# Optimization experiments

Hardware: AMD Instinct MI355X
Metric: run time of the kernel (lower is better)

The kernel has to match this reference:

```python
import jax, jax.numpy as jnp
import numpy as np
import math

N_HEADS = 4
N_KV_GROUPS = 1
HEAD_DIM = 256
SLIDING_WINDOW = 512
ROPE_BASE = 1000000.0
EPS = 1e-6


def _rmsnorm(x, gamma):
    # normalize over last dim (head_dim), torch nn.RMSNorm semantics
    ms = jnp.mean(jnp.square(x), axis=-1, keepdims=True)
    return x * jax.lax.rsqrt(ms + EPS) * gamma


def _rope_tables(T, head_dim, dtype):
    inv_freq = 1.0 / (ROPE_BASE ** (jnp.arange(0, head_dim, 2, dtype=jnp.float32) / head_dim))
    t = jnp.arange(T, dtype=jnp.float32)
    freqs = jnp.outer(t, inv_freq)          # [T, head_dim/2]
    return jnp.cos(freqs).astype(dtype), jnp.sin(freqs).astype(dtype)


def _apply_rope(x, cos, sin):
    # x: [B, T, H, hd]; cos/sin: [T, hd/2] broadcast as [1, T, 1, hd/2]
    x0 = x[..., 0::2]
    x1 = x[..., 1::2]
    c = cos[None, :, None, :]
    s = sin[None, :, None, :]
    even = x0 * c - x1 * s
    odd = x0 * s + x1 * c
    return jnp.stack((even, odd), axis=-1).reshape(x.shape)


def setup_inputs() -> dict:
    key = jax.random.key(0)
    ks = jax.random.split(key, 5)
    B, T, C = 2, 4096, 1024
    scale = 0.02
    return {
        "x": jax.random.normal(ks[0], (B, T, C), dtype=jnp.float32),
        "Wq": jax.random.normal(ks[1], (C, C), dtype=jnp.float32) * scale,
        "Wk": jax.random.normal(ks[2], (N_KV_GROUPS * HEAD_DIM, C), dtype=jnp.float32) * scale,
        "Wv": jax.random.normal(ks[3], (N_KV_GROUPS * HEAD_DIM, C), dtype=jnp.float32) * scale,
        "Wo": jax.random.normal(ks[4], (C, C), dtype=jnp.float32) * scale,
        "q_gamma": jnp.ones((HEAD_DIM,), dtype=jnp.float32),
        "k_gamma": jnp.ones((HEAD_DIM,), dtype=jnp.float32),
    }


def reference(x, Wq, Wk, Wv, Wo, q_gamma, k_gamma):
    B, T, C = x.shape
    H, G, hd = N_HEADS, N_KV_GROUPS, HEAD_DIM
    rep = H // G

    q = (x @ Wq.T).reshape(B, T, H, hd)
    k = (x @ Wk.T).reshape(B, T, G, hd)
    v = (x @ Wv.T).reshape(B, T, G, hd)

    q = _rmsnorm(q, q_gamma)
    k = _rmsnorm(k, k_gamma)

    cos, sin = _rope_tables(T, hd, q.dtype)
    q = _apply_rope(q, cos, sin)
    k = _apply_rope(k, cos, sin)

    q = q.transpose(0, 2, 1, 3)                 # [B, H, T, hd]
    k = k.transpose(0, 2, 1, 3)                 # [B, G, T, hd]
    v = v.transpose(0, 2, 1, 3)
    k = jnp.repeat(k, rep, axis=1)              # [B, H, T, hd]
    v = jnp.repeat(v, rep, axis=1)

    scores = jnp.einsum("bhqd,bhkd->bhqk", q, k) / math.sqrt(hd)
    i = jnp.arange(T)[:, None]
    j = jnp.arange(T)[None, :]
    allowed = (j <= i) & (j >= i - SLIDING_WINDOW)   # causal sliding window
    scores = jnp.where(allowed, scores, -jnp.inf)
    attn = jax.nn.softmax(scores, axis=-1)
    out = jnp.einsum("bhqk,bhkd->bhqd", attn, v)     # [B, H, T, hd]
    out = out.transpose(0, 2, 1, 3).reshape(B, T, C)
    return out @ Wo.T
```

## Files before the change

kernel.cpp:

```cpp
#include <hip/hip_runtime.h>
#include <cstdint>
#include <cstddef>

#define T_SEQ 4096
#define NB    2
#define CDIM  1024
#define HD    256
#define NH    4

typedef __attribute__((ext_vector_type(8))) __bf16 bf16x8;
typedef __attribute__((ext_vector_type(4))) __bf16 bf16x4;
typedef __attribute__((ext_vector_type(4))) float  floatx4;

__device__ __forceinline__ floatx4 mfma16(bf16x8 a, bf16x8 b, floatx4 c) {
  return __builtin_amdgcn_mfma_f32_16x16x32_bf16(a, b, c, 0, 0, 0);
}

__device__ __forceinline__ void gl2lds16(const void* g, void* l) {
  __builtin_amdgcn_global_load_lds(
      (__attribute__((address_space(1))) void*)g,
      (__attribute__((address_space(3))) void*)l, 16, 0, 0);
}

__global__ void cvt_f32_bf16(const float* __restrict__ in,
                             __bf16* __restrict__ out, int n4) {
  int i = blockIdx.x * 256 + threadIdx.x;
  if (i < n4) {
    float4 v = ((const float4*)in)[i];
    bf16x4 o;
    o[0] = (__bf16)v.x; o[1] = (__bf16)v.y; o[2] = (__bf16)v.z; o[3] = (__bf16)v.w;
    *(bf16x4*)&out[(size_t)i * 4] = o;
  }
}

template <typename OutT>
__global__ __launch_bounds__(256) void gemm_bt(const __bf16* __restrict__ A,
                                               const __bf16* __restrict__ B,
                                               OutT* __restrict__ C,
                                               int M, int N, int K) {
  __shared__ __bf16 As[128 * 64];
  __shared__ __bf16 Bs[128 * 64];
  const int tid  = threadIdx.x;
  const int lane = tid & 63;
  const int wave = tid >> 6;
  const int wm = wave >> 1, wn = wave & 1;
  const int lrow = lane & 15, quad = lane >> 4;
  const int bm = blockIdx.y, bn = blockIdx.x;

  const __bf16* gA = A + (size_t)(bm * 128) * K;
  const __bf16* gB = B + (size_t)(bn * 128) * K;
  const int arow = tid >> 3;
  const int acol = ((tid & 7) ^ ((tid >> 3) & 7)) * 8;
  const int l7 = lrow & 7;

  floatx4 acc[4][4] = {};

  for (int kt = 0; kt < K; kt += 64) {
#pragma unroll
    for (int i = 0; i < 4; ++i)
      gl2lds16(gA + (size_t)(i * 32 + arow) * K + kt + acol, &As[i * 2048 + tid * 8]);
#pragma unroll
    for (int i = 0; i < 4; ++i)
      gl2lds16(gB + (size_t)(i * 32 + arow) * K + kt + acol, &Bs[i * 2048 + tid * 8]);
    __syncthreads();
#pragma unroll
    for (int kk = 0; kk < 2; ++kk) {
      bf16x8 af[4], bfr[4];
#pragma unroll
      for (int mi = 0; mi < 4; ++mi)
        af[mi] = *(const bf16x8*)&As[(wm * 64 + mi * 16 + lrow) * 64 +
                                     ((kk * 4 + quad) ^ l7) * 8];
#pragma unroll
      for (int ni = 0; ni < 4; ++ni)
        bfr[ni] = *(const bf16x8*)&Bs[(wn * 64 + ni * 16 + lrow) * 64 +
                                      ((kk * 4 + quad) ^ l7) * 8];
#pragma unroll
      for (int mi = 0; mi < 4; ++mi)
#pragma unroll
        for (int ni = 0; ni < 4; ++ni)
          acc[mi][ni] = mfma16(af[mi], bfr[ni], acc[mi][ni]);
    }
    __syncthreads();
  }

  const int row0 = bm * 128 + wm * 64;
  const int col0 = bn * 128 + wn * 64;
#pragma unroll
  for (int mi = 0; mi < 4; ++mi)
#pragma unroll
    for (int ni = 0; ni < 4; ++ni)
#pragma unroll
      for (int r = 0; r < 4; ++r) {
        int row = row0 + mi * 16 + quad * 4 + r;
        int col = col0 + ni * 16 + lrow;
        C[(size_t)row * N + col] = (OutT)acc[mi][ni][r];
      }
}

__global__ __launch_bounds__(256) void rmsrope(const __bf16* __restrict__ qkv,
                                               const float* __restrict__ qg,
                                               const float* __restrict__ kg,
                                               __bf16* __restrict__ qr,
                                               __bf16* __restrict__ kr,
                                               __bf16* __restrict__ vt) {
  __shared__ __bf16 Ls[64 * 256];
  if (blockIdx.x >= 10240) {
    const int vb = blockIdx.x - 10240;
    const int b = vb >> 6, tt = vb & 63;
    const int tid = threadIdx.x;
    const __bf16* src = qkv + ((size_t)(b * 4096 + tt * 64)) * 1536 + 1280;
#pragma unroll
    for (int i = 0; i < 8; ++i)
      gl2lds16(src + (size_t)(i * 8 + (tid >> 5)) * 1536 + (tid & 31) * 8,
               &Ls[i * 2048 + tid * 8]);
    __syncthreads();
    __bf16 buf[64];
#pragma unroll
    for (int i = 0; i < 64; ++i) buf[i] = Ls[i * 256 + tid];
    __bf16* dst = vt + ((size_t)(b * 256 + tid)) * T_SEQ + tt * 64;
#pragma unroll
    for (int i = 0; i < 8; ++i)
      *(bf16x8*)&dst[i * 8] = *(const bf16x8*)&buf[i * 8];
    return;
  }

  const int inst = blockIdx.x * 4 + (threadIdx.x >> 6);
  const int lane = threadIdx.x & 63;
  const int row = inst / 5, which = inst - row * 5;
  const int b = row >> 12, t = row & 4095;

  const int srcoff = (which < 4) ? which * 256 : 1024;
  const __bf16* src = qkv + (size_t)row * 1536 + srcoff;
  bf16x4 xv = *(const bf16x4*)&src[lane * 4];

  float x0 = (float)xv[0], x1 = (float)xv[1], x2 = (float)xv[2], x3 = (float)xv[3];
  float ss = x0 * x0 + x1 * x1 + x2 * x2 + x3 * x3;
#pragma unroll
  for (int off = 32; off >= 1; off >>= 1) ss += __shfl_xor(ss, off);
  const float rms = rsqrtf(ss * (1.0f / 256.0f) + 1e-6f);

  const float* g = (which < 4) ? qg : kg;
  const float4 gv = *(const float4*)&g[lane * 4];
  float y0 = x0 * rms * gv.x, y1 = x1 * rms * gv.y;
  float y2 = x2 * rms * gv.z, y3 = x3 * rms * gv.w;

  const float c_log2 = -19.931568569324174f / 128.0f;
  int p0 = lane * 2, p1 = lane * 2 + 1;
  float a0 = (float)t * exp2f((float)p0 * c_log2);
  float a1 = (float)t * exp2f((float)p1 * c_log2);
  float s0, c0, s1, c1;
  sincosf(a0, &s0, &c0);
  sincosf(a1, &s1, &c1);
  bf16x4 ov;
  ov[0] = (__bf16)(y0 * c0 - y1 * s0);
  ov[1] = (__bf16)(y0 * s0 + y1 * c0);
  ov[2] = (__bf16)(y2 * c1 - y3 * s1);
  ov[3] = (__bf16)(y2 * s1 + y3 * c1);

  __bf16* dst = (which < 4)
      ? qr + ((size_t)((b * NH + which) * T_SEQ) + t) * 256
      : kr + ((size_t)(b * T_SEQ) + t) * 256;
  *(bf16x4*)&dst[lane * 4] = ov;
}

__global__ __launch_bounds__(256, 2) void attn(const __bf16* __restrict__ qr,
                                               const __bf16* __restrict__ kr,
                                               const __bf16* __restrict__ vt,
                                               __bf16* __restrict__ ao) {
  __shared__ __bf16 Ks[64 * 256];
  __shared__ __bf16 Ps[64 * 64];

  const int bid = blockIdx.x;
  const int qi = bid & 63, h = (bid >> 6) & 3, b = bid >> 8;
  const int tid = threadIdx.x, wave = tid >> 6, lane = tid & 63;
  const int wq = wave & 1, wk = wave >> 1;
  const int lrow = lane & 15, quad = lane >> 4;
  const int l7 = lrow & 7;

  const __bf16* Q = qr + (size_t)((b * NH + h) * T_SEQ) * 256;
  const __bf16* K = kr + (size_t)(b * T_SEQ) * 256;
  const __bf16* V = vt + (size_t)(b * 256) * T_SEQ;

  const int qbase = qi * 64;

  bf16x8 qf[2][8];
#pragma unroll
  for (int qt = 0; qt < 2; ++qt)
#pragma unroll
    for (int c = 0; c < 8; ++c)
      qf[qt][c] = *(const bf16x8*)&Q[(size_t)(qbase + wq * 32 + qt * 16 + lrow) * 256 +
                                     c * 32 + quad * 8];

  bf16x8 onesv;
#pragma unroll
  for (int j = 0; j < 8; ++j) onesv[j] = (__bf16)1.0f;

  floatx4 o[2][8] = {};
  floatx4 lm[2] = {};

  const int jt0 = (qi >= 8) ? qi - 8 : 0;
  const int jt1 = qi;

  {
    const __bf16* Kt = K + (size_t)(jt0 * 64) * 256;
#pragma unroll
    for (int i = 0; i < 8; ++i)
      gl2lds16(Kt + (size_t)(i * 8 + (tid >> 5)) * 256 +
                   ((tid & 31) ^ ((tid >> 5) & 7)) * 8,
               &Ks[i * 2048 + tid * 8]);
  }

  for (int jt = jt0; jt <= jt1; ++jt) {
    __syncthreads();

    floatx4 s[2][2] = {};
#pragma unroll
    for (int c = 0; c < 8; ++c)
#pragma unroll
      for (int k16 = 0; k16 < 2; ++k16) {
        bf16x8 kf = *(const bf16x8*)&Ks[(wk * 32 + k16 * 16 + lrow) * 256 +
                                        ((c * 4 + quad) ^ l7) * 8];
#pragma unroll
        for (int qt = 0; qt < 2; ++qt)
          s[k16][qt] = mfma16(kf, qf[qt][c], s[k16][qt]);
      }

    const bool full = (jt < qi) && (jt >= qi - 7);

    const float C1 = 0.09016844005556021f;
    const float C2 = 23.083120654223415f;
#pragma unroll
    for (int k16 = 0; k16 < 2; ++k16)
#pragma unroll
      for (int qt = 0; qt < 2; ++qt) {
        bf16x4 pk;
#pragma unroll
        for (int r = 0; r < 4; ++r) {
          float v = s[k16][qt][r];
          if (!full) {
            const int jk = jt * 64 + wk * 32 + k16 * 16 + quad * 4 + r;
            const int iq = qbase + wq * 32 + qt * 16 + lrow;
            v = ((jk <= iq) && (jk + 512 >= iq)) ? v : -1e30f;
          }
          pk[r] = (__bf16)exp2f(v * C1 - C2);
        }
        const int q = wq * 32 + qt * 16 + lrow;
        const int chunk = (wk * 4 + k16 * 2 + (quad >> 1)) ^ l7;
        *(bf16x4*)((char*)Ps + q * 128 + chunk * 16 + (quad & 1) * 8) = pk;
      }
    __syncthreads();

    if (jt < jt1) {
      const __bf16* Kt = K + (size_t)((jt + 1) * 64) * 256;
#pragma unroll
      for (int i = 0; i < 8; ++i)
        gl2lds16(Kt + (size_t)(i * 8 + (tid >> 5)) * 256 +
                     ((tid & 31) ^ ((tid >> 5) & 7)) * 8,
                 &Ks[i * 2048 + tid * 8]);
    }

    bf16x8 pf[2][2];
#pragma unroll
    for (int qt = 0; qt < 2; ++qt)
#pragma unroll
      for (int kc = 0; kc < 2; ++kc) {
        const int q = wq * 32 + qt * 16 + lrow;
        pf[qt][kc] = *(const bf16x8*)((char*)Ps + q * 128 +
                                      ((kc * 4 + quad) ^ l7) * 16);
      }

#pragma unroll
    for (int qt = 0; qt < 2; ++qt) {
      lm[qt] = mfma16(pf[qt][0], onesv, lm[qt]);
      lm[qt] = mfma16(pf[qt][1], onesv, lm[qt]);
    }

#pragma unroll
    for (int n = 0; n < 8; ++n)
#pragma unroll
      for (int kc = 0; kc < 2; ++kc) {
        bf16x8 vf = *(const bf16x8*)&V[(size_t)(wk * 128 + n * 16 + lrow) * T_SEQ +
                                       jt * 64 + kc * 32 + quad * 8];
        o[0][n] = mfma16(pf[0][kc], vf, o[0][n]);
        o[1][n] = mfma16(pf[1][kc], vf, o[1][n]);
      }
  }

#pragma unroll
  for (int qt = 0; qt < 2; ++qt)
#pragma unroll
    for (int r = 0; r < 4; ++r) {
      const float rl = 1.0f / lm[qt][r];
      const int tg = qbase + wq * 32 + qt * 16 + quad * 4 + r;
#pragma unroll
      for (int n = 0; n < 8; ++n)
        ao[((size_t)(b * T_SEQ + tg)) * CDIM + h * 256 + wk * 128 + n * 16 + lrow] =
            (__bf16)(o[qt][n][r] * rl);
    }
}

extern "C" void kernel_launch(void* const* d_in, const int* in_sizes, int n_in,
                              void* d_out, int out_size, void* d_ws, size_t ws_size,
                              hipStream_t stream) {
  const float* x  = (const float*)d_in[0];
  const float* Wq = (const float*)d_in[1];
  const float* Wk = (const float*)d_in[2];
  const float* Wv = (const float*)d_in[3];
  const float* Wo = (const float*)d_in[4];
  const float* qg = (const float*)d_in[5];
  const float* kg = (const float*)d_in[6];
  float* out = (float*)d_out;

  const size_t M = (size_t)NB * T_SEQ;
  char* ws = (char*)d_ws;
  __bf16* xb  = (__bf16*)ws; ws += M * CDIM * 2;
  __bf16* wb  = (__bf16*)ws; ws += (size_t)1536 * CDIM * 2;
  __bf16* wob = (__bf16*)ws; ws += (size_t)CDIM * CDIM * 2;
  __bf16* qkv = (__bf16*)ws; ws += M * 1536 * 2;
  __bf16* qr  = (__bf16*)ws; ws += M * CDIM * 2;
  __bf16* kr  = (__bf16*)ws; ws += M * HD * 2;
  __bf16* vt  = (__bf16*)ws; ws += M * HD * 2;
  __bf16* ao  = (__bf16*)ws;

  cvt_f32_bf16<<<8192, 256, 0, stream>>>(x, xb, 2097152);
  cvt_f32_bf16<<<1024, 256, 0, stream>>>(Wq, wb, 262144);
  cvt_f32_bf16<<<256,  256, 0, stream>>>(Wk, wb + 1024 * 1024, 65536);
  cvt_f32_bf16<<<256,  256, 0, stream>>>(Wv, wb + 1280 * 1024, 65536);
  cvt_f32_bf16<<<1024, 256, 0, stream>>>(Wo, wob, 262144);

  gemm_bt<__bf16><<<dim3(12, 64), 256, 0, stream>>>(xb, wb, qkv, 8192, 1536, 1024);

  rmsrope<<<10368, 256, 0, stream>>>(qkv, qg, kg, qr, kr, vt);

  attn<<<NB * NH * (T_SEQ / 64), 256, 0, stream>>>(qr, kr, vt, ao);

  gemm_bt<float><<<dim3(8, 64), 256, 0, stream>>>(ao, wob, out, 8192, 1024, 1024);
}
```

Before: 235.8 us.

## Double-buffer attention K/P tiles, prefetch V early, fuse conversions, fast sincos

The attention kernel now double-buffers the K and P tiles in LDS and prefetches K two tiles ahead. V fragments are loaded into registers at the top of each iteration so global latency overlaps the QK MFMAs. The five fp32-to-bf16 conversion launches are merged into one kernel, and the RoPE sincosf calls are replaced with the __sinf/__cosf intrinsics. The costs are doubled LDS use, higher register pressure from holding vf, and reduced trig accuracy at large angles (t up to 4096).

```diff
diff --git a/kernel.cpp b/kernel.cpp
--- a/kernel.cpp
+++ b/kernel.cpp
@@ -22,15 +22,27 @@
       (__attribute__((address_space(3))) void*)l, 16, 0, 0);
 }
 
-__global__ void cvt_f32_bf16(const float* __restrict__ in,
-                             __bf16* __restrict__ out, int n4) {
+__global__ __launch_bounds__(256) void cvt_all(const float* __restrict__ x,
+                                               const float* __restrict__ wq,
+                                               const float* __restrict__ wk,
+                                               const float* __restrict__ wv,
+                                               const float* __restrict__ wo,
+                                               __bf16* __restrict__ xb,
+                                               __bf16* __restrict__ wb,
+                                               __bf16* __restrict__ wob) {
   int i = blockIdx.x * 256 + threadIdx.x;
-  if (i < n4) {
-    float4 v = ((const float4*)in)[i];
-    bf16x4 o;
-    o[0] = (__bf16)v.x; o[1] = (__bf16)v.y; o[2] = (__bf16)v.z; o[3] = (__bf16)v.w;
-    *(bf16x4*)&out[(size_t)i * 4] = o;
-  }
+  const float* src;
+  __bf16* dst;
+  int off;
+  if (i < 2097152)      { src = x;  dst = xb;            off = i; }
+  else if (i < 2359296) { src = wq; dst = wb;            off = i - 2097152; }
+  else if (i < 2424832) { src = wk; dst = wb + 1048576;  off = i - 2359296; }
+  else if (i < 2490368) { src = wv; dst = wb + 1310720;  off = i - 2424832; }
+  else                  { src = wo; dst = wob;           off = i - 2490368; }
+  float4 v = ((const float4*)src)[off];
+  bf16x4 o;
+  o[0] = (__bf16)v.x; o[1] = (__bf16)v.y; o[2] = (__bf16)v.z; o[3] = (__bf16)v.w;
+  *(bf16x4*)&dst[(size_t)off * 4] = o;
 }
 
 template <typename OutT>
@@ -148,9 +160,8 @@
   int p0 = lane * 2, p1 = lane * 2 + 1;
   float a0 = (float)t * exp2f((float)p0 * c_log2);
   float a1 = (float)t * exp2f((float)p1 * c_log2);
-  float s0, c0, s1, c1;
-  sincosf(a0, &s0, &c0);
-  sincosf(a1, &s1, &c1);
+  float s0 = __sinf(a0), c0 = __cosf(a0);
+  float s1 = __sinf(a1), c1 = __cosf(a1);
   bf16x4 ov;
   ov[0] = (__bf16)(y0 * c0 - y1 * s0);
   ov[1] = (__bf16)(y0 * s0 + y1 * c0);
@@ -167,8 +178,8 @@
                                                const __bf16* __restrict__ kr,
                                                const __bf16* __restrict__ vt,
                                                __bf16* __restrict__ ao) {
-  __shared__ __bf16 Ks[64 * 256];
-  __shared__ __bf16 Ps[64 * 64];
+  __shared__ __bf16 Ks[2][64 * 256];
+  __shared__ __bf16 Ps[2][64 * 64];
 
   const int bid = blockIdx.x;
   const int qi = bid & 63, h = (bid >> 6) & 3, b = bid >> 8;
@@ -207,18 +218,36 @@
     for (int i = 0; i < 8; ++i)
       gl2lds16(Kt + (size_t)(i * 8 + (tid >> 5)) * 256 +
                    ((tid & 31) ^ ((tid >> 5) & 7)) * 8,
-               &Ks[i * 2048 + tid * 8]);
-  }
+               &Ks[jt0 & 1][i * 2048 + tid * 8]);
+  }
+  if (jt1 > jt0) {
+    const __bf16* Kt = K + (size_t)((jt0 + 1) * 64) * 256;
+#pragma unroll
+    for (int i = 0; i < 8; ++i)
+      gl2lds16(Kt + (size_t)(i * 8 + (tid >> 5)) * 256 +
+                   ((tid & 31) ^ ((tid >> 5) & 7)) * 8,
+               &Ks[(jt0 + 1) & 1][i * 2048 + tid * 8]);
+  }
+  __syncthreads();
 
   for (int jt = jt0; jt <= jt1; ++jt) {
-    __syncthreads();
+    const __bf16* Kb = Ks[jt & 1];
+    __bf16* Pb = Ps[jt & 1];
+
+    bf16x8 vf[8][2];
+#pragma unroll
+    for (int n = 0; n < 8; ++n)
+#pragma unroll
+      for (int kc = 0; kc < 2; ++kc)
+        vf[n][kc] = *(const bf16x8*)&V[(size_t)(wk * 128 + n * 16 + lrow) * T_SEQ +
+                                       jt * 64 + kc * 32 + quad * 8];
 
     floatx4 s[2][2] = {};
 #pragma unroll
     for (int c = 0; c < 8; ++c)
 #pragma unroll
       for (int k16 = 0; k16 < 2; ++k16) {
-        bf16x8 kf = *(const bf16x8*)&Ks[(wk * 32 + k16 * 16 + lrow) * 256 +
+        bf16x8 kf = *(const bf16x8*)&Kb[(wk * 32 + k16 * 16 + lrow) * 256 +
                                         ((c * 4 + quad) ^ l7) * 8];
 #pragma unroll
         for (int qt = 0; qt < 2; ++qt)
@@ -246,17 +275,17 @@
         }
         const int q = wq * 32 + qt * 16 + lrow;
         const int chunk = (wk * 4 + k16 * 2 + (quad >> 1)) ^ l7;
-        *(bf16x4*)((char*)Ps + q * 128 + chunk * 16 + (quad & 1) * 8) = pk;
+        *(bf16x4*)((char*)Pb + q * 128 + chunk * 16 + (quad & 1) * 8) = pk;
       }
     __syncthreads();
 
-    if (jt < jt1) {
-      const __bf16* Kt = K + (size_t)((jt + 1) * 64) * 256;
+    if (jt + 2 <= jt1) {
+      const __bf16* Kt = K + (size_t)((jt + 2) * 64) * 256;
 #pragma unroll
       for (int i = 0; i < 8; ++i)
         gl2lds16(Kt + (size_t)(i * 8 + (tid >> 5)) * 256 +
                      ((tid & 31) ^ ((tid >> 5) & 7)) * 8,
-                 &Ks[i * 2048 + tid * 8]);
+                 &Ks[jt & 1][i * 2048 + tid * 8]);
     }
 
     bf16x8 pf[2][2];
@@ -265,7 +294,7 @@
 #pragma unroll
       for (int kc = 0; kc < 2; ++kc) {
         const int q = wq * 32 + qt * 16 + lrow;
-        pf[qt][kc] = *(const bf16x8*)((char*)Ps + q * 128 +
+        pf[qt][kc] = *(const bf16x8*)((char*)Pb + q * 128 +
                                       ((kc * 4 + quad) ^ l7) * 16);
       }
 
@@ -279,10 +308,8 @@
     for (int n = 0; n < 8; ++n)
 #pragma unroll
       for (int kc = 0; kc < 2; ++kc) {
-        bf16x8 vf = *(const bf16x8*)&V[(size_t)(wk * 128 + n * 16 + lrow) * T_SEQ +
-                                       jt * 64 + kc * 32 + quad * 8];
-        o[0][n] = mfma16(pf[0][kc], vf, o[0][n]);
-        o[1][n] = mfma16(pf[1][kc], vf, o[1][n]);
+        o[0][n] = mfma16(pf[0][kc], vf[n][kc], o[0][n]);
+        o[1][n] = mfma16(pf[1][kc], vf[n][kc], o[1][n]);
       }
   }
 
@@ -322,11 +349,7 @@
   __bf16* vt  = (__bf16*)ws; ws += M * HD * 2;
   __bf16* ao  = (__bf16*)ws;
 
-  cvt_f32_bf16<<<8192, 256, 0, stream>>>(x, xb, 2097152);
-  cvt_f32_bf16<<<1024, 256, 0, stream>>>(Wq, wb, 262144);
-  cvt_f32_bf16<<<256,  256, 0, stream>>>(Wk, wb + 1024 * 1024, 65536);
-  cvt_f32_bf16<<<256,  256, 0, stream>>>(Wv, wb + 1280 * 1024, 65536);
-  cvt_f32_bf16<<<1024, 256, 0, stream>>>(Wo, wob, 262144);
+  cvt_all<<<10752, 256, 0, stream>>>(x, Wq, Wk, Wv, Wo, xb, wb, wob);
 
   gemm_bt<__bf16><<<dim3(12, 64), 256, 0, stream>>>(xb, wb, qkv, 8192, 1536, 1024);
 
```

Result: slower. 250.8 us (+6.3%).
